# Kernel optimization log

Hardware: AMD Instinct MI355X
Metric: run time of the kernel (lower is better)

## Reference

```python
import jax, jax.numpy as jnp
import numpy as np

B, R, H, IN, L = 8, 128, 256, 512, 3
NH, DH = 4, H // 4  # attention heads


def _layernorm(x, g, b, eps=1e-5):
    mu = jnp.mean(x, axis=-1, keepdims=True)
    var = jnp.mean(jnp.square(x - mu), axis=-1, keepdims=True)
    return (x - mu) * jax.lax.rsqrt(var + eps) * g + b


def setup_inputs() -> dict:
    key = jax.random.key(0)
    ks = iter(jax.random.split(key, 40))
    s = 0.02
    d = {}
    d['x'] = jax.random.normal(next(ks), (B, IN), jnp.float32)
    d['We'] = jax.random.normal(next(ks), (IN, H), jnp.float32) * s
    d['be'] = jnp.zeros((H,), jnp.float32)
    # per-graph-layer params, stacked along leading L axis
    d['msg_W1'] = jax.random.normal(next(ks), (L, 2 * H, H), jnp.float32) * s
    d['msg_b1'] = jnp.zeros((L, H), jnp.float32)
    d['msg_W2'] = jax.random.normal(next(ks), (L, H, H), jnp.float32) * s
    d['msg_b2'] = jnp.zeros((L, H), jnp.float32)
    d['upd_W1'] = jax.random.normal(next(ks), (L, 2 * H, H), jnp.float32) * s
    d['upd_b1'] = jnp.zeros((L, H), jnp.float32)
    d['upd_W2'] = jax.random.normal(next(ks), (L, H, H), jnp.float32) * s
    d['upd_b2'] = jnp.zeros((L, H), jnp.float32)
    d['ln_g'] = jnp.ones((L, H), jnp.float32)
    d['ln_b'] = jnp.zeros((L, H), jnp.float32)
    d['rule_adj'] = jax.random.normal(next(ks), (R, R), jnp.float32)
    # multihead attention (4 heads)
    d['Wq'] = jax.random.normal(next(ks), (H, H), jnp.float32) * s
    d['bq'] = jnp.zeros((H,), jnp.float32)
    d['Wk'] = jax.random.normal(next(ks), (H, H), jnp.float32) * s
    d['bk'] = jnp.zeros((H,), jnp.float32)
    d['Wv'] = jax.random.normal(next(ks), (H, H), jnp.float32) * s
    d['bv'] = jnp.zeros((H,), jnp.float32)
    d['Wo'] = jax.random.normal(next(ks), (H, H), jnp.float32) * s
    d['bo'] = jnp.zeros((H,), jnp.float32)
    # readout MLP -> num_rules logits
    d['ro_W1'] = jax.random.normal(next(ks), (H, H), jnp.float32) * s
    d['ro_b1'] = jnp.zeros((H,), jnp.float32)
    d['ro_W2'] = jax.random.normal(next(ks), (H, R), jnp.float32) * s
    d['ro_b2'] = jnp.zeros((R,), jnp.float32)
    return d


def reference(x, We, be, msg_W1, msg_b1, msg_W2, msg_b2,
              upd_W1, upd_b1, upd_W2, upd_b2, ln_g, ln_b, rule_adj,
              Wq, bq, Wk, bk, Wv, bv, Wo, bo,
              ro_W1, ro_b1, ro_W2, ro_b2):
    # node encoder, broadcast to all rule-graph nodes: [B,R,H]
    h0 = x @ We + be
    h = jnp.broadcast_to(h0[:, None, :], (B, R, H))
    # rule adjacency with self-edges excluded (loop used i != j)
    A = jax.nn.sigmoid(rule_adj) * (1.0 - jnp.eye(R, dtype=rule_adj.dtype))  # [R,R]
    for l in range(L):
        # message_net(cat(h_i, h_j)) = relu(h_i@W1a + h_j@W1b + b1)@W2 + b2
        W1a, W1b = msg_W1[l][:H], msg_W1[l][H:]
        a = h @ W1a   # [B,R,H] (receiver i part)
        bb = h @ W1b  # [B,R,H] (sender j part)
        pre = jax.nn.relu(a[:, :, None, :] + bb[:, None, :, :] + msg_b1[l])  # [B,R,R,H]
        m = pre @ msg_W2[l] + msg_b2[l]  # [B,R,R,H] message from j to i
        agg = jnp.einsum('bijh,ij->bih', m, A)  # weighted sum over senders j
        # update_net(cat(h, agg))
        Wu1a, Wu1b = upd_W1[l][:H], upd_W1[l][H:]
        u = jax.nn.relu(h @ Wu1a + agg @ Wu1b + upd_b1[l]) @ upd_W2[l] + upd_b2[l]
        h = _layernorm(h + u, ln_g[l], ln_b[l])
    # multihead self-attention over nodes
    q = (h @ Wq + bq).reshape(B, R, NH, DH)
    k = (h @ Wk + bk).reshape(B, R, NH, DH)
    v = (h @ Wv + bv).reshape(B, R, NH, DH)
    logits = jnp.einsum('bqhd,bkhd->bhqk', q, k) / jnp.sqrt(jnp.float32(DH))
    attn = jax.nn.softmax(logits, axis=-1)
    pooled = jnp.einsum('bhqk,bkhd->bqhd', attn, v).reshape(B, R, H) @ Wo + bo
    g = jnp.mean(pooled, axis=1)  # [B,H]
    rule_logits = jax.nn.relu(g @ ro_W1 + ro_b1) @ ro_W2 + ro_b2
    rule_probabilities = jax.nn.softmax(rule_logits, axis=-1)  # [B,R]
    return rule_probabilities
```

## Files before the change

### kernel.cpp

```cpp
#include <hip/hip_runtime.h>
#include <math.h>

constexpr int NB  = 8;
constexpr int NR  = 128;
constexpr int HID = 256;
constexpr int NIN = 512;
constexpr int DHD = 64;
constexpr size_t SZ = (size_t)NB * NR * HID;

struct KP {
    const float *x, *We, *be, *msg_W1, *msg_b1, *msg_W2, *msg_b2;
    const float *upd_W1, *upd_b1, *upd_W2, *upd_b2, *ln_g, *ln_b, *rule_adj;
    const float *Wq, *bq, *Wk, *bk, *Wv, *bv, *Wo, *bo, *ro_W1, *ro_b1, *ro_W2, *ro_b2;
    float* out;
    float *N0, *N1, *N2;
    float *aB, *bbB, *p1B;
    float *aA, *bbA, *p1A;
    float *W2u, *mb2u, *Aw, *rsum;
    float *mW1s;
    float *h0g;
    float *gacc;
    float *scratch;
};

__device__ __forceinline__ void gemm_core(
    float (&As)[16][68], float (&Bs)[16][64], int m0, int n0,
    const float* __restrict__ A, const float* __restrict__ B,
    float (&acc)[4][4])
{
    int tid = threadIdx.x;
    int ty = tid >> 4, tx = tid & 15;
    int arow = tid >> 2, acol = (tid & 3) << 2;
    int brow = tid >> 4, bcol = (tid & 15) << 2;
    int m = m0 + arow;

    float4 av = *(const float4*)&A[(size_t)m * HID + acol];
    float4 bv = *(const float4*)&B[(size_t)brow * HID + n0 + bcol];

    for (int k0 = 0; k0 < HID; k0 += 16) {
        As[acol + 0][arow] = av.x;
        As[acol + 1][arow] = av.y;
        As[acol + 2][arow] = av.z;
        As[acol + 3][arow] = av.w;
        *(float4*)&Bs[brow][bcol] = bv;
        __syncthreads();
        if (k0 + 16 < HID) {
            av = *(const float4*)&A[(size_t)m * HID + k0 + 16 + acol];
            bv = *(const float4*)&B[(size_t)(k0 + 16 + brow) * HID + n0 + bcol];
        }
#pragma unroll
        for (int kk = 0; kk < 16; ++kk) {
            float4 af = *(const float4*)&As[kk][ty << 2];
            float4 bf = *(const float4*)&Bs[kk][tx << 2];
            float a_[4] = {af.x, af.y, af.z, af.w};
            float b_[4] = {bf.x, bf.y, bf.z, bf.w};
#pragma unroll
            for (int i = 0; i < 4; ++i)
#pragma unroll
                for (int j = 0; j < 4; ++j) acc[i][j] += a_[i] * b_[j];
        }
        __syncthreads();
    }
}

__device__ __forceinline__ void gemv256w(
    const float* xs, const float* __restrict__ W,
    const float* __restrict__ bias, int relu, float* ys, float* red)
{
    int tid = threadIdx.x;
    int w = tid >> 6, l = tid & 63;
    float4 acc = {0.f, 0.f, 0.f, 0.f};
    const float* Wp = W + (size_t)(w * 64) * HID + l * 4;
    const float* xp = xs + w * 64;
#pragma unroll 16
    for (int kk = 0; kk < 64; ++kk) {
        float xv = xp[kk];
        float4 wv = *(const float4*)(Wp + (size_t)kk * HID);
        acc.x += xv * wv.x; acc.y += xv * wv.y;
        acc.z += xv * wv.z; acc.w += xv * wv.w;
    }
    *(float4*)&red[w * 256 + l * 4] = acc;
    __syncthreads();
    float v = red[tid] + red[256 + tid] + red[512 + tid] + red[768 + tid];
    if (bias) v += bias[tid];
    if (relu) v = fmaxf(v, 0.0f);
    ys[tid] = v;
    __syncthreads();
}

__device__ __forceinline__ void rows4_q(
    const float (&rows)[4][HID], const float* __restrict__ W,
    int col, int q, float o[4])
{
    o[0] = o[1] = o[2] = o[3] = 0.f;
    int kb = q * 64;
#pragma unroll 4
    for (int k0 = 0; k0 < 64; k0 += 4) {
        int k = kb + k0;
        float w0 = W[(size_t)(k + 0) * HID + col];
        float w1 = W[(size_t)(k + 1) * HID + col];
        float w2 = W[(size_t)(k + 2) * HID + col];
        float w3 = W[(size_t)(k + 3) * HID + col];
#pragma unroll
        for (int ii = 0; ii < 4; ++ii) {
            float4 rv = *(const float4*)&rows[ii][k];
            o[ii] += rv.x * w0 + rv.y * w1 + rv.z * w2 + rv.w * w3;
        }
    }
}

__device__ __forceinline__ float gemv_q(
    const float* xs, const float* __restrict__ W, int col, int q)
{
    float o = 0.f;
    int kb = q * 64;
#pragma unroll 8
    for (int k = 0; k < 64; ++k)
        o += xs[kb + k] * W[(size_t)(kb + k) * HID + col];
    return o;
}

__device__ __forceinline__ void ln_stats4_q(
    float (&sred)[4][4][2], float (&mi)[4][2], const float v[4], int q)
{
    if (q == 0) {
        int w = threadIdx.x >> 6, l = threadIdx.x & 63;
        float s[4], qq[4];
#pragma unroll
        for (int ii = 0; ii < 4; ++ii) { s[ii] = v[ii]; qq[ii] = v[ii] * v[ii]; }
#pragma unroll
        for (int off = 32; off; off >>= 1) {
#pragma unroll
            for (int ii = 0; ii < 4; ++ii) {
                s[ii] += __shfl_xor(s[ii], off);
                qq[ii] += __shfl_xor(qq[ii], off);
            }
        }
        if (l == 0) {
#pragma unroll
            for (int ii = 0; ii < 4; ++ii) { sred[w][ii][0] = s[ii]; sred[w][ii][1] = qq[ii]; }
        }
    }
    __syncthreads();
    if (threadIdx.x < 4) {
        int r = threadIdx.x;
        float ss = sred[0][r][0] + sred[1][r][0] + sred[2][r][0] + sred[3][r][0];
        float qq = sred[0][r][1] + sred[1][r][1] + sred[2][r][1] + sred[3][r][1];
        float mu = ss * (1.0f / HID);
        mi[r][0] = mu;
        mi[r][1] = rsqrtf(qq * (1.0f / HID) - mu * mu + 1e-5f);
    }
    __syncthreads();
}

__global__ __launch_bounds__(256) void setup0_kernel(KP P) {
    __shared__ union {
        struct { float As[16][68]; float Bs[16][64]; } g;
        struct { float xs[NIN]; float part[8][32]; } e;
    } L;
    int blk = blockIdx.x;
    int t = threadIdx.x;

    if (blk < 32) {
        int rr = blk * 4 + (t >> 6);
        int l = t & 63;
        float s_loc = 0.f;
#pragma unroll
        for (int rep = 0; rep < 2; ++rep) {
            int j = l + rep * 64;
            float xv = P.rule_adj[rr * NR + j];
            float sg = 1.0f / (1.0f + expf(-xv));
            if (j == rr) sg = 0.0f;
            P.Aw[rr * NR + j] = sg;
            s_loc += sg;
        }
#pragma unroll
        for (int off = 32; off; off >>= 1) s_loc += __shfl_xor(s_loc, off);
        if (l == 0) P.rsum[rr] = s_loc;
    } else if (blk < 80) {
        int idx = blk - 32, l2 = idx >> 4, t16 = idx & 15;
        int m0 = (t16 >> 2) * 64, n0 = (t16 & 3) * 64;
        float acc[4][4] = {};
        gemm_core(L.g.As, L.g.Bs, m0, n0,
                  P.msg_W2 + (size_t)l2 * HID * HID,
                  P.upd_W1 + (size_t)l2 * 2 * HID * HID + (size_t)HID * HID,
                  acc);
        int ty = t >> 4, tx = t & 15;
        float* C = P.W2u + (size_t)l2 * HID * HID;
#pragma unroll
        for (int i = 0; i < 4; ++i) {
            int m = m0 + (ty << 2) + i, n = n0 + (tx << 2);
            float4 o = {acc[i][0], acc[i][1], acc[i][2], acc[i][3]};
            *(float4*)&C[(size_t)m * HID + n] = o;
        }
    } else if (blk < 83) {
        int l2 = blk - 80;
        const float* b2v = P.msg_b2 + l2 * HID;
        const float* Bm = P.upd_W1 + (size_t)l2 * 2 * HID * HID + (size_t)HID * HID;
        float acc = 0.f;
#pragma unroll 4
        for (int k = 0; k < HID; ++k) acc += b2v[k] * Bm[(size_t)k * HID + t];
        P.mb2u[l2 * HID + t] = acc;
    } else if (blk < 147) {
        int idx = blk - 83;
        int b = idx >> 3, s = idx & 7;
        L.e.xs[t]       = P.x[b * NIN + t];
        L.e.xs[256 + t] = P.x[b * NIN + 256 + t];
        __syncthreads();
        int c = t & 31, seg = t >> 5;
        int col = s * 32 + c;
        const float* Wp = P.We + (size_t)(seg * 64) * HID + col;
        const float* xp = L.e.xs + seg * 64;
        float acc = 0.f;
#pragma unroll 16
        for (int k = 0; k < 64; ++k) acc += xp[k] * Wp[(size_t)k * HID];
        L.e.part[seg][c] = acc;
        __syncthreads();
        if (t < 32) {
            float v = 0.f;
#pragma unroll
            for (int sg = 0; sg < 8; ++sg) v += L.e.part[sg][t];
            int cc = s * 32 + t;
            P.h0g[b * HID + cc] = v + P.be[cc];
        }
    } else if (blk < 163) {
        int base = (blk - 147) * 4096;
        for (int i = t; i < 4096; i += 256) {
            int o = base + i;
            P.mW1s[o] = P.msg_W1[o] + P.msg_W1[65536 + o];
        }
    } else {
        int pfid = blk - 163, npf = 256 - 163;
        const float* arr[11] = {P.We, P.msg_W1, P.msg_W2, P.upd_W1, P.upd_W2,
                                P.Wq, P.Wk, P.Wv, P.Wo, P.ro_W1, P.ro_W2};
        const int n4[11] = {32768, 98304, 49152, 98304, 49152,
                            16384, 16384, 16384, 16384, 16384, 8192};
        float s = 0.f;
        for (int a = 0; a < 11; ++a) {
            const float4* p4 = (const float4*)arr[a];
            for (int i = pfid * 256 + t; i < n4[a]; i += npf * 256) {
                float4 v = p4[i];
                s += v.x + v.y + v.z + v.w;
            }
        }
        if (s == 1.0e37f) P.scratch[pfid] = s;
    }
}

__global__ __launch_bounds__(1024) void layer0p_kernel(KP P) {
    __shared__ float h0s[HID], p0s[HID], c0s[HID], c1s[HID];
    __shared__ float u1s[4][HID];
    __shared__ float nrm[4][HID];
    __shared__ float part4[4][4][HID];
    __shared__ float sred[4][4][2];
    __shared__ float mi[4][2];
    int blk = blockIdx.x;
    int m0 = blk * 4;
    int b = m0 >> 7, i0 = m0 & 127;
    int t = threadIdx.x;
    int col = t & 255, q = t >> 8;

    if (q == 0) h0s[col] = P.h0g[b * HID + col];
    __syncthreads();

    part4[q][0][col] = gemv_q(h0s, P.upd_W1, col, q);
    part4[q][1][col] = gemv_q(h0s, P.mW1s, col, q);
    __syncthreads();
    if (q == 0) {
        c0s[col] = part4[0][0][col] + part4[1][0][col] + part4[2][0][col] + part4[3][0][col];
        float pv = part4[0][1][col] + part4[1][1][col] + part4[2][1][col] + part4[3][1][col];
        p0s[col] = fmaxf(pv + P.msg_b1[col], 0.0f);
    }
    __syncthreads();
    part4[q][0][col] = gemv_q(p0s, P.W2u, col, q);
    __syncthreads();
    if (q == 0) {
        c1s[col] = part4[0][0][col] + part4[1][0][col] + part4[2][0][col] + part4[3][0][col]
                 + P.mb2u[col];
        float ubv = P.upd_b1[col];
#pragma unroll
        for (int ii = 0; ii < 4; ++ii)
            u1s[ii][col] = fmaxf(c0s[col] + P.rsum[i0 + ii] * c1s[col] + ubv, 0.0f);
    }
    __syncthreads();

    float o[4];
    rows4_q(u1s, P.upd_W2, col, q, o);
#pragma unroll
    for (int ii = 0; ii < 4; ++ii) part4[q][ii][col] = o[ii];
    __syncthreads();
    float v[4] = {0.f, 0.f, 0.f, 0.f};
    if (q == 0) {
        float h0v = h0s[col] + P.upd_b2[col];
#pragma unroll
        for (int ii = 0; ii < 4; ++ii)
            v[ii] = part4[0][ii][col] + part4[1][ii][col] + part4[2][ii][col]
                  + part4[3][ii][col] + h0v;
    }
    ln_stats4_q(sred, mi, v, q);
    if (q == 0) {
        float gv = P.ln_g[col], btv = P.ln_b[col];
#pragma unroll
        for (int ii = 0; ii < 4; ++ii) {
            float nv = (v[ii] - mi[ii][0]) * mi[ii][1] * gv + btv;
            nrm[ii][col] = nv;
            P.N0[(size_t)(m0 + ii) * HID + col] = nv;
        }
    }
    __syncthreads();

    const float* mW1a1 = P.msg_W1 + (size_t)1 * 2 * HID * HID;
    const float* uW1a1 = P.upd_W1 + (size_t)1 * 2 * HID * HID;
    const float* pw[3] = {mW1a1, mW1a1 + (size_t)HID * HID, uW1a1};
    float* po[3] = {P.aB, P.bbB, P.p1B};
#pragma unroll
    for (int p = 0; p < 3; ++p) {
        rows4_q(nrm, pw[p], col, q, o);
#pragma unroll
        for (int ii = 0; ii < 4; ++ii) part4[q][ii][col] = o[ii];
        __syncthreads();
        if (q == 0) {
#pragma unroll
            for (int ii = 0; ii < 4; ++ii)
                po[p][(size_t)(m0 + ii) * HID + col] =
                    part4[0][ii][col] + part4[1][ii][col] +
                    part4[2][ii][col] + part4[3][ii][col];
        }
        __syncthreads();
    }
}

__global__ __launch_bounds__(1024) void aggproj_kernel(
    const float* __restrict__ a, const float* __restrict__ bbv,
    const float* __restrict__ mb1, const float* __restrict__ Aw,
    const float* __restrict__ rsumv,
    const float* __restrict__ P1, const float* __restrict__ W2u,
    const float* __restrict__ mb2u, const float* __restrict__ ub1,
    const float* __restrict__ uW2, const float* __restrict__ ub2,
    const float* __restrict__ Nprev, const float* __restrict__ lng,
    const float* __restrict__ lnb, float* __restrict__ Nout,
    const float* __restrict__ pw0, const float* __restrict__ pb0, float* __restrict__ o0,
    const float* __restrict__ pw1, const float* __restrict__ pb1, float* __restrict__ o1,
    const float* __restrict__ pw2, const float* __restrict__ pb2, float* __restrict__ o2,
    float* __restrict__ gzero)
{
    __shared__ float ap[4][HID];
    __shared__ float u1s[4][HID];
    __shared__ float nrm[4][HID];
    __shared__ float awr[4][NR];
    __shared__ float part4[4][4][HID];
    __shared__ float sred[4][4][2];
    __shared__ float mi[4][2];
    int blk = blockIdx.x;
    int b  = blk >> 5;
    int i0 = (blk & 31) * 4;
    int m0 = b * NR + i0;
    int t  = threadIdx.x;
    int col = t & 255, q = t >> 8;

    if (gzero && blk == 0 && q == 0) {
#pragma unroll
        for (int i = 0; i < 8; ++i) gzero[i * 256 + col] = 0.f;
    }

    if (t < 512) awr[t >> 7][t & 127] = Aw[(i0 + (t >> 7)) * NR + (t & 127)];

    float bias = mb1[col];
    float ai[4];
#pragma unroll
    for (int ii = 0; ii < 4; ++ii)
        ai[ii] = a[(size_t)(m0 + ii) * HID + col] + bias;
    __syncthreads();

    {
        float acc[4] = {0.f, 0.f, 0.f, 0.f};
        const float* bbb = &bbv[(size_t)b * NR * HID + col];
        int jb = q * 32;
#pragma unroll 4
        for (int j = 0; j < 32; ++j) {
            float bj = bbb[(size_t)(jb + j) * HID];
#pragma unroll
            for (int ii = 0; ii < 4; ++ii) {
                float pre = fmaxf(ai[ii] + bj, 0.0f);
                acc[ii] += awr[ii][jb + j] * pre;
            }
        }
#pragma unroll
        for (int ii = 0; ii < 4; ++ii) part4[q][ii][col] = acc[ii];
        __syncthreads();
        if (q == 0) {
#pragma unroll
            for (int ii = 0; ii < 4; ++ii)
                ap[ii][col] = part4[0][ii][col] + part4[1][ii][col]
                            + part4[2][ii][col] + part4[3][ii][col];
        }
        __syncthreads();
    }

    {
        float o[4];
        rows4_q(ap, W2u, col, q, o);
#pragma unroll
        for (int ii = 0; ii < 4; ++ii) part4[q][ii][col] = o[ii];
        __syncthreads();
        if (q == 0) {
            float mbv = mb2u[col], ubv = ub1[col];
#pragma unroll
            for (int ii = 0; ii < 4; ++ii) {
                float w2f = part4[0][ii][col] + part4[1][ii][col]
                          + part4[2][ii][col] + part4[3][ii][col];
                float vv = w2f + P1[(size_t)(m0 + ii) * HID + col]
                         + rsumv[i0 + ii] * mbv + ubv;
                u1s[ii][col] = fmaxf(vv, 0.0f);
            }
        }
        __syncthreads();
    }

    {
        float o[4];
        rows4_q(u1s, uW2, col, q, o);
#pragma unroll
        for (int ii = 0; ii < 4; ++ii) part4[q][ii][col] = o[ii];
        __syncthreads();
        float v[4] = {0.f, 0.f, 0.f, 0.f};
        if (q == 0) {
            float ub2v = ub2[col];
#pragma unroll
            for (int ii = 0; ii < 4; ++ii) {
                float uf = part4[0][ii][col] + part4[1][ii][col]
                         + part4[2][ii][col] + part4[3][ii][col];
                v[ii] = Nprev[(size_t)(m0 + ii) * HID + col] + uf + ub2v;
            }
        }
        ln_stats4_q(sred, mi, v, q);
        if (q == 0) {
            float gv = lng[col], btv = lnb[col];
#pragma unroll
            for (int ii = 0; ii < 4; ++ii) {
                float nv = (v[ii] - mi[ii][0]) * mi[ii][1] * gv + btv;
                nrm[ii][col] = nv;
                Nout[(size_t)(m0 + ii) * HID + col] = nv;
            }
        }
        __syncthreads();
    }

    {
        const float* pw[3] = {pw0, pw1, pw2};
        const float* pb[3] = {pb0, pb1, pb2};
        float* po[3] = {o0, o1, o2};
#pragma unroll
        for (int p = 0; p < 3; ++p) {
            float o[4];
            rows4_q(nrm, pw[p], col, q, o);
#pragma unroll
            for (int ii = 0; ii < 4; ++ii) part4[q][ii][col] = o[ii];
            __syncthreads();
            if (q == 0) {
                float pbv = pb[p] ? pb[p][col] : 0.f;
#pragma unroll
                for (int ii = 0; ii < 4; ++ii)
                    po[p][(size_t)(m0 + ii) * HID + col] =
                        part4[0][ii][col] + part4[1][ii][col] +
                        part4[2][ii][col] + part4[3][ii][col] + pbv;
            }
            __syncthreads();
        }
    }
}

__global__ __launch_bounds__(256) void attention_kernel(
    const float* __restrict__ q, const float* __restrict__ k,
    const float* __restrict__ v, float* __restrict__ gacc)
{
    __shared__ struct { float KhT[64][128]; float S[16][128]; float qs[16][64]; } L;
    int blk = blockIdx.x;
    int bh = blk >> 3, ig = blk & 7;
    int b = bh >> 2, hd = bh & 3;
    int i0 = ig * 16;
    int t = threadIdx.x;
    const float* qg = q + ((size_t)b * NR) * HID + hd * DHD;
    const float* kg = k + ((size_t)b * NR) * HID + hd * DHD;
    const float* vg = v + ((size_t)b * NR) * HID + hd * DHD;

    {
        int j = t >> 1, half = t & 1;
        const float* krow = kg + (size_t)j * HID + half * 32;
#pragma unroll
        for (int c = 0; c < 32; c += 4) {
            float4 kv = *(const float4*)(krow + c);
            L.KhT[half * 32 + c + 0][j] = kv.x;
            L.KhT[half * 32 + c + 1][j] = kv.y;
            L.KhT[half * 32 + c + 2][j] = kv.z;
            L.KhT[half * 32 + c + 3][j] = kv.w;
        }
    }
    {
        int ii = t >> 4, d0 = (t & 15) * 4;
        *(float4*)&L.qs[ii][d0] = *(const float4*)(qg + (size_t)(i0 + ii) * HID + d0);
    }
    __syncthreads();
    {
        int j = t & 127, ii2 = t >> 7;
        float acc[8] = {0.f,0.f,0.f,0.f,0.f,0.f,0.f,0.f};
#pragma unroll 4
        for (int d = 0; d < 64; ++d) {
            float kv = L.KhT[d][j];
#pragma unroll
            for (int ii = 0; ii < 8; ++ii) acc[ii] += L.qs[ii2 * 8 + ii][d] * kv;
        }
#pragma unroll
        for (int ii = 0; ii < 8; ++ii) L.S[ii2 * 8 + ii][j] = acc[ii] * 0.125f;
    }
    __syncthreads();
    {
        int w = t >> 6, l = t & 63;
#pragma unroll
        for (int r = w * 4; r < w * 4 + 4; ++r) {
            float e0 = L.S[r][l], e1 = L.S[r][l + 64];
            float mx = fmaxf(e0, e1);
#pragma unroll
            for (int off = 32; off; off >>= 1) mx = fmaxf(mx, __shfl_xor(mx, off));
            e0 = expf(e0 - mx); e1 = expf(e1 - mx);
            float sm = e0 + e1;
#pragma unroll
            for (int off = 32; off; off >>= 1) sm += __shfl_xor(sm, off);
            float inv = 1.0f / sm;
            L.S[r][l] = e0 * inv; L.S[r][l + 64] = e1 * inv;
        }
    }
    __syncthreads();
    {
        int d = t & 63, ir = t >> 6;
        float accv[4] = {0.f, 0.f, 0.f, 0.f};
        const float* vp = vg + d;
#pragma unroll 8
        for (int j = 0; j < NR; ++j) {
            float vv = vp[(size_t)j * HID];
#pragma unroll
            for (int p = 0; p < 4; ++p) accv[p] += L.S[p * 4 + ir][j] * vv;
        }
        float s = accv[0] + accv[1] + accv[2] + accv[3];
        atomicAdd(&gacc[b * HID + hd * DHD + d], s);
    }
}

__global__ __launch_bounds__(256) void tailf_kernel(KP P) {
    __shared__ float v0[HID], v1[HID], v2[HID];
    __shared__ float red[1024];
    int b = blockIdx.x;
    int t = threadIdx.x;
    int w = t >> 6, l = t & 63;

    v0[t] = P.gacc[b * HID + t] * (1.0f / NR);
    __syncthreads();
    gemv256w(v0, P.Wo, P.bo, 0, v1, red);
    gemv256w(v1, P.ro_W1, P.ro_b1, 1, v2, red);

    {
        float2 acc = {0.f, 0.f};
        const float* Wp = P.ro_W2 + (size_t)(w * 64) * NR + l * 2;
        const float* xp = v2 + w * 64;
#pragma unroll 8
        for (int kk = 0; kk < 64; ++kk) {
            float xv = xp[kk];
            float2 wv = *(const float2*)(Wp + (size_t)kk * NR);
            acc.x += xv * wv.x; acc.y += xv * wv.y;
        }
        *(float2*)&red[w * 128 + l * 2] = acc;
        __syncthreads();
    }
    float logit = -1e30f;
    if (t < NR) logit = red[t] + red[128 + t] + red[256 + t] + red[384 + t] + P.ro_b2[t];
    __syncthreads();
    float m = logit;
#pragma unroll
    for (int off = 32; off; off >>= 1) m = fmaxf(m, __shfl_xor(m, off));
    if (l == 0) red[w] = m;
    __syncthreads();
    m = fmaxf(red[0], red[1]);
    float e = (t < NR) ? expf(logit - m) : 0.0f;
    float ssum = e;
#pragma unroll
    for (int off = 32; off; off >>= 1) ssum += __shfl_xor(ssum, off);
    if (l == 0) red[4 + w] = ssum;
    __syncthreads();
    float tot = red[4] + red[5];
    if (t < NR) P.out[b * NR + t] = e / tot;
}

extern "C" void kernel_launch(void* const* d_in, const int* in_sizes, int n_in,
                              void* d_out, int out_size, void* d_ws, size_t ws_size,
                              hipStream_t stream)
{
    KP P;
    P.x        = (const float*)d_in[0];
    P.We       = (const float*)d_in[1];
    P.be       = (const float*)d_in[2];
    P.msg_W1   = (const float*)d_in[3];
    P.msg_b1   = (const float*)d_in[4];
    P.msg_W2   = (const float*)d_in[5];
    P.msg_b2   = (const float*)d_in[6];
    P.upd_W1   = (const float*)d_in[7];
    P.upd_b1   = (const float*)d_in[8];
    P.upd_W2   = (const float*)d_in[9];
    P.upd_b2   = (const float*)d_in[10];
    P.ln_g     = (const float*)d_in[11];
    P.ln_b     = (const float*)d_in[12];
    P.rule_adj = (const float*)d_in[13];
    P.Wq       = (const float*)d_in[14];
    P.bq       = (const float*)d_in[15];
    P.Wk       = (const float*)d_in[16];
    P.bk       = (const float*)d_in[17];
    P.Wv       = (const float*)d_in[18];
    P.bv       = (const float*)d_in[19];
    P.Wo       = (const float*)d_in[20];
    P.bo       = (const float*)d_in[21];
    P.ro_W1    = (const float*)d_in[22];
    P.ro_b1    = (const float*)d_in[23];
    P.ro_W2    = (const float*)d_in[24];
    P.ro_b2    = (const float*)d_in[25];
    P.out      = (float*)d_out;

    float* b0 = (float*)d_ws;
    P.N0     = b0;  b0 += SZ;
    P.N1     = b0;  b0 += SZ;
    P.N2     = b0;  b0 += SZ;
    P.aB     = b0;  b0 += SZ;
    P.bbB    = b0;  b0 += SZ;
    P.p1B    = b0;  b0 += SZ;
    P.aA     = b0;  b0 += SZ;
    P.bbA    = b0;  b0 += SZ;
    P.p1A    = b0;  b0 += SZ;
    P.W2u    = b0;  b0 += 3 * HID * HID;
    P.mb2u   = b0;  b0 += 3 * HID;
    P.mW1s   = b0;  b0 += HID * HID;
    P.Aw     = b0;  b0 += NR * NR;
    P.rsum   = b0;  b0 += NR;
    P.h0g    = b0;  b0 += NB * HID;
    P.gacc   = b0;  b0 += NB * HID;
    P.scratch= b0;  b0 += 256;

    setup0_kernel<<<dim3(256), 256, 0, stream>>>(P);

    layer0p_kernel<<<dim3(256), 1024, 0, stream>>>(P);

    {
        const int l = 1;
        const float* mW1a2 = P.msg_W1 + (size_t)2 * 2 * HID * HID;
        const float* uW1a2 = P.upd_W1 + (size_t)2 * 2 * HID * HID;
        aggproj_kernel<<<dim3(256), 1024, 0, stream>>>(
            P.aB, P.bbB, P.msg_b1 + (size_t)l * HID, P.Aw, P.rsum,
            P.p1B, P.W2u + (size_t)l * HID * HID, P.mb2u + l * HID,
            P.upd_b1 + (size_t)l * HID,
            P.upd_W2 + (size_t)l * HID * HID, P.upd_b2 + (size_t)l * HID,
            P.N0, P.ln_g + (size_t)l * HID, P.ln_b + (size_t)l * HID, P.N1,
            mW1a2, nullptr, P.aA,
            mW1a2 + (size_t)HID * HID, nullptr, P.bbA,
            uW1a2, nullptr, P.p1A,
            nullptr);
    }

    {
        const int l = 2;
        aggproj_kernel<<<dim3(256), 1024, 0, stream>>>(
            P.aA, P.bbA, P.msg_b1 + (size_t)l * HID, P.Aw, P.rsum,
            P.p1A, P.W2u + (size_t)l * HID * HID, P.mb2u + l * HID,
            P.upd_b1 + (size_t)l * HID,
            P.upd_W2 + (size_t)l * HID * HID, P.upd_b2 + (size_t)l * HID,
            P.N1, P.ln_g + (size_t)l * HID, P.ln_b + (size_t)l * HID, P.N2,
            P.Wq, P.bq, P.aB,
            P.Wk, P.bk, P.bbB,
            P.Wv, P.bv, P.p1B,
            P.gacc);
    }

    attention_kernel<<<dim3(256), 256, 0, stream>>>(P.aB, P.bbB, P.p1B, P.gacc);

    tailf_kernel<<<dim3(8), 256, 0, stream>>>(P);
}
```

Measured before the change: 228.1 us.

## Retile layer kernels to 2 rows x 2 columns per thread with fused projections

Restructures layer0p and aggproj kernels from 4 rows per 1024-thread block to 2 rows per 512-thread block, doubling grid size to 512 blocks. Each thread now computes two adjacent columns using float2 weight loads, and the three output projections are computed in a single pass sharing row loads, with one barrier instead of three. All threads now take part in reductions and layernorm instead of only a quarter of them. The aim is better occupancy across CUs and fewer barriers. The cost is that each weight matrix is reused over only 2 rows per block, so weight traffic from cache doubles.

Result: slower. 293.2 us (+28.5%).

```diff
diff --git a/kernel.cpp b/kernel.cpp
--- a/kernel.cpp
+++ b/kernel.cpp
@@ -88,69 +88,74 @@
     __syncthreads();
 }
 
-__device__ __forceinline__ void rows4_q(
-    const float (&rows)[4][HID], const float* __restrict__ W,
-    int col, int q, float o[4])
-{
-    o[0] = o[1] = o[2] = o[3] = 0.f;
+__device__ __forceinline__ void rows2x2_q(
+    const float (&rows)[2][HID], const float* __restrict__ W,
+    int col2, int q, float o[2][2])
+{
+    o[0][0] = o[0][1] = o[1][0] = o[1][1] = 0.f;
+    int kb = q * 64;
+#pragma unroll 8
+    for (int k0 = 0; k0 < 64; k0 += 4) {
+        int k = kb + k0;
+        float2 w0 = *(const float2*)&W[(size_t)(k + 0) * HID + col2];
+        float2 w1 = *(const float2*)&W[(size_t)(k + 1) * HID + col2];
+        float2 w2 = *(const float2*)&W[(size_t)(k + 2) * HID + col2];
+        float2 w3 = *(const float2*)&W[(size_t)(k + 3) * HID + col2];
+#pragma unroll
+        for (int ii = 0; ii < 2; ++ii) {
+            float4 rv = *(const float4*)&rows[ii][k];
+            o[ii][0] += rv.x * w0.x + rv.y * w1.x + rv.z * w2.x + rv.w * w3.x;
+            o[ii][1] += rv.x * w0.y + rv.y * w1.y + rv.z * w2.y + rv.w * w3.y;
+        }
+    }
+}
+
+__device__ __forceinline__ void rows2x2_q3(
+    const float (&rows)[2][HID],
+    const float* __restrict__ W0, const float* __restrict__ W1,
+    const float* __restrict__ W2m, int col2, int q, float o[3][2][2])
+{
+#pragma unroll
+    for (int p = 0; p < 3; ++p)
+        o[p][0][0] = o[p][0][1] = o[p][1][0] = o[p][1][1] = 0.f;
     int kb = q * 64;
 #pragma unroll 4
     for (int k0 = 0; k0 < 64; k0 += 4) {
         int k = kb + k0;
-        float w0 = W[(size_t)(k + 0) * HID + col];
-        float w1 = W[(size_t)(k + 1) * HID + col];
-        float w2 = W[(size_t)(k + 2) * HID + col];
-        float w3 = W[(size_t)(k + 3) * HID + col];
-#pragma unroll
-        for (int ii = 0; ii < 4; ++ii) {
-            float4 rv = *(const float4*)&rows[ii][k];
-            o[ii] += rv.x * w0 + rv.y * w1 + rv.z * w2 + rv.w * w3;
-        }
-    }
-}
-
-__device__ __forceinline__ float gemv_q(
-    const float* xs, const float* __restrict__ W, int col, int q)
-{
-    float o = 0.f;
+        float4 r0 = *(const float4*)&rows[0][k];
+        float4 r1 = *(const float4*)&rows[1][k];
+        const float* Wp[3] = {W0, W1, W2m};
+#pragma unroll
+        for (int p = 0; p < 3; ++p) {
+            const float* W = Wp[p];
+            float2 w0 = *(const float2*)&W[(size_t)(k + 0) * HID + col2];
+            float2 w1 = *(const float2*)&W[(size_t)(k + 1) * HID + col2];
+            float2 w2 = *(const float2*)&W[(size_t)(k + 2) * HID + col2];
+            float2 w3 = *(const float2*)&W[(size_t)(k + 3) * HID + col2];
+            o[p][0][0] += r0.x * w0.x + r0.y * w1.x + r0.z * w2.x + r0.w * w3.x;
+            o[p][0][1] += r0.x * w0.y + r0.y * w1.y + r0.z * w2.y + r0.w * w3.y;
+            o[p][1][0] += r1.x * w0.x + r1.y * w1.x + r1.z * w2.x + r1.w * w3.x;
+            o[p][1][1] += r1.x * w0.y + r1.y * w1.y + r1.z * w2.y + r1.w * w3.y;
+        }
+    }
+}
+
+__device__ __forceinline__ void row1x2_q(
+    const float* xs, const float* __restrict__ W, int col2, int q, float o[2])
+{
+    o[0] = o[1] = 0.f;
     int kb = q * 64;
 #pragma unroll 8
-    for (int k = 0; k < 64; ++k)
-        o += xs[kb + k] * W[(size_t)(kb + k) * HID + col];
-    return o;
-}
-
-__device__ __forceinline__ void ln_stats4_q(
-    float (&sred)[4][4][2], float (&mi)[4][2], const float v[4], int q)
-{
-    if (q == 0) {
-        int w = threadIdx.x >> 6, l = threadIdx.x & 63;
-        float s[4], qq[4];
-#pragma unroll
-        for (int ii = 0; ii < 4; ++ii) { s[ii] = v[ii]; qq[ii] = v[ii] * v[ii]; }
-#pragma unroll
-        for (int off = 32; off; off >>= 1) {
-#pragma unroll
-            for (int ii = 0; ii < 4; ++ii) {
-                s[ii] += __shfl_xor(s[ii], off);
-                qq[ii] += __shfl_xor(qq[ii], off);
-            }
-        }
-        if (l == 0) {
-#pragma unroll
-            for (int ii = 0; ii < 4; ++ii) { sred[w][ii][0] = s[ii]; sred[w][ii][1] = qq[ii]; }
-        }
-    }
-    __syncthreads();
-    if (threadIdx.x < 4) {
-        int r = threadIdx.x;
-        float ss = sred[0][r][0] + sred[1][r][0] + sred[2][r][0] + sred[3][r][0];
-        float qq = sred[0][r][1] + sred[1][r][1] + sred[2][r][1] + sred[3][r][1];
-        float mu = ss * (1.0f / HID);
-        mi[r][0] = mu;
-        mi[r][1] = rsqrtf(qq * (1.0f / HID) - mu * mu + 1e-5f);
-    }
-    __syncthreads();
+    for (int k0 = 0; k0 < 64; k0 += 4) {
+        int k = kb + k0;
+        float4 xv = *(const float4*)&xs[k];
+        float2 w0 = *(const float2*)&W[(size_t)(k + 0) * HID + col2];
+        float2 w1 = *(const float2*)&W[(size_t)(k + 1) * HID + col2];
+        float2 w2 = *(const float2*)&W[(size_t)(k + 2) * HID + col2];
+        float2 w3 = *(const float2*)&W[(size_t)(k + 3) * HID + col2];
+        o[0] += xv.x * w0.x + xv.y * w1.x + xv.z * w2.x + xv.w * w3.x;
+        o[1] += xv.x * w0.y + xv.y * w1.y + xv.z * w2.y + xv.w * w3.y;
+    }
 }
 
 __global__ __launch_bounds__(256) void setup0_kernel(KP P) {
@@ -247,90 +252,103 @@
     }
 }
 
-__global__ __launch_bounds__(1024) void layer0p_kernel(KP P) {
+__global__ __launch_bounds__(512) void layer0p_kernel(KP P) {
     __shared__ float h0s[HID], p0s[HID], c0s[HID], c1s[HID];
-    __shared__ float u1s[4][HID];
-    __shared__ float nrm[4][HID];
-    __shared__ float part4[4][4][HID];
-    __shared__ float sred[4][4][2];
-    __shared__ float mi[4][2];
+    __shared__ float u1s[2][HID];
+    __shared__ float nrm[2][HID];
+    __shared__ float part3[3][4][2][HID];
+    __shared__ float sred[8][2];
+    __shared__ float mi[2][2];
     int blk = blockIdx.x;
-    int m0 = blk * 4;
+    int m0 = blk * 2;
     int b = m0 >> 7, i0 = m0 & 127;
     int t = threadIdx.x;
-    int col = t & 255, q = t >> 8;
-
-    if (q == 0) h0s[col] = P.h0g[b * HID + col];
-    __syncthreads();
-
-    part4[q][0][col] = gemv_q(h0s, P.upd_W1, col, q);
-    part4[q][1][col] = gemv_q(h0s, P.mW1s, col, q);
-    __syncthreads();
-    if (q == 0) {
-        c0s[col] = part4[0][0][col] + part4[1][0][col] + part4[2][0][col] + part4[3][0][col];
-        float pv = part4[0][1][col] + part4[1][1][col] + part4[2][1][col] + part4[3][1][col];
-        p0s[col] = fmaxf(pv + P.msg_b1[col], 0.0f);
-    }
-    __syncthreads();
-    part4[q][0][col] = gemv_q(p0s, P.W2u, col, q);
-    __syncthreads();
-    if (q == 0) {
-        c1s[col] = part4[0][0][col] + part4[1][0][col] + part4[2][0][col] + part4[3][0][col]
-                 + P.mb2u[col];
-        float ubv = P.upd_b1[col];
-#pragma unroll
-        for (int ii = 0; ii < 4; ++ii)
-            u1s[ii][col] = fmaxf(c0s[col] + P.rsum[i0 + ii] * c1s[col] + ubv, 0.0f);
-    }
-    __syncthreads();
-
-    float o[4];
-    rows4_q(u1s, P.upd_W2, col, q, o);
-#pragma unroll
-    for (int ii = 0; ii < 4; ++ii) part4[q][ii][col] = o[ii];
-    __syncthreads();
-    float v[4] = {0.f, 0.f, 0.f, 0.f};
-    if (q == 0) {
-        float h0v = h0s[col] + P.upd_b2[col];
-#pragma unroll
-        for (int ii = 0; ii < 4; ++ii)
-            v[ii] = part4[0][ii][col] + part4[1][ii][col] + part4[2][ii][col]
-                  + part4[3][ii][col] + h0v;
-    }
-    ln_stats4_q(sred, mi, v, q);
-    if (q == 0) {
-        float gv = P.ln_g[col], btv = P.ln_b[col];
-#pragma unroll
-        for (int ii = 0; ii < 4; ++ii) {
-            float nv = (v[ii] - mi[ii][0]) * mi[ii][1] * gv + btv;
-            nrm[ii][col] = nv;
-            P.N0[(size_t)(m0 + ii) * HID + col] = nv;
-        }
-    }
-    __syncthreads();
-
-    const float* mW1a1 = P.msg_W1 + (size_t)1 * 2 * HID * HID;
-    const float* uW1a1 = P.upd_W1 + (size_t)1 * 2 * HID * HID;
-    const float* pw[3] = {mW1a1, mW1a1 + (size_t)HID * HID, uW1a1};
-    float* po[3] = {P.aB, P.bbB, P.p1B};
-#pragma unroll
-    for (int p = 0; p < 3; ++p) {
-        rows4_q(nrm, pw[p], col, q, o);
-#pragma unroll
-        for (int ii = 0; ii < 4; ++ii) part4[q][ii][col] = o[ii];
-        __syncthreads();
-        if (q == 0) {
-#pragma unroll
-            for (int ii = 0; ii < 4; ++ii)
-                po[p][(size_t)(m0 + ii) * HID + col] =
-                    part4[0][ii][col] + part4[1][ii][col] +
-                    part4[2][ii][col] + part4[3][ii][col];
-        }
-        __syncthreads();
-    }
-}
-
-__global__ __launch_bounds__(1024) void aggproj_kernel(
+    int c2 = t & 127, q = t >> 7, col2 = c2 * 2;
+    int r = t >> 8, c = t & 255;
+
+    if (t < 256) h0s[t] = P.h0g[b * HID + t];
+    __syncthreads();
+
+    {
+        float o0v[2], o1v[2];
+        row1x2_q(h0s, P.upd_W1, col2, q, o0v);
+        row1x2_q(h0s, P.mW1s, col2, q, o1v);
+        *(float2*)&part3[0][q][0][col2] = make_float2(o0v[0], o0v[1]);
+        *(float2*)&part3[0][q][1][col2] = make_float2(o1v[0], o1v[1]);
+        __syncthreads();
+        float s = part3[0][0][r][c] + part3[0][1][r][c]
+                + part3[0][2][r][c] + part3[0][3][r][c];
+        if (r == 0) c0s[c] = s;
+        else        p0s[c] = fmaxf(s + P.msg_b1[c], 0.0f);
+        __syncthreads();
+    }
+    {
+        float ov[2];
+        row1x2_q(p0s, P.W2u, col2, q, ov);
+        *(float2*)&part3[0][q][0][col2] = make_float2(ov[0], ov[1]);
+        __syncthreads();
+        if (t < 256)
+            c1s[t] = part3[0][0][0][t] + part3[0][1][0][t]
+                   + part3[0][2][0][t] + part3[0][3][0][t] + P.mb2u[t];
+        __syncthreads();
+    }
+    u1s[r][c] = fmaxf(c0s[c] + P.rsum[i0 + r] * c1s[c] + P.upd_b1[c], 0.0f);
+    __syncthreads();
+
+    {
+        float o[2][2];
+        rows2x2_q(u1s, P.upd_W2, col2, q, o);
+#pragma unroll
+        for (int ii = 0; ii < 2; ++ii)
+            *(float2*)&part3[0][q][ii][col2] = make_float2(o[ii][0], o[ii][1]);
+        __syncthreads();
+        float uf = part3[0][0][r][c] + part3[0][1][r][c]
+                 + part3[0][2][r][c] + part3[0][3][r][c];
+        float v = h0s[c] + uf + P.upd_b2[c];
+        float s = v, qq = v * v;
+#pragma unroll
+        for (int off = 32; off; off >>= 1) {
+            s += __shfl_xor(s, off); qq += __shfl_xor(qq, off);
+        }
+        int wid = t >> 6;
+        if ((t & 63) == 0) { sred[wid][0] = s; sred[wid][1] = qq; }
+        __syncthreads();
+        if (t < 2) {
+            float ss = sred[4*t][0] + sred[4*t+1][0] + sred[4*t+2][0] + sred[4*t+3][0];
+            float q2 = sred[4*t][1] + sred[4*t+1][1] + sred[4*t+2][1] + sred[4*t+3][1];
+            float mu = ss * (1.0f / HID);
+            mi[t][0] = mu;
+            mi[t][1] = rsqrtf(q2 * (1.0f / HID) - mu * mu + 1e-5f);
+        }
+        __syncthreads();
+        float nv = (v - mi[r][0]) * mi[r][1] * P.ln_g[c] + P.ln_b[c];
+        nrm[r][c] = nv;
+        P.N0[(size_t)(m0 + r) * HID + c] = nv;
+        __syncthreads();
+    }
+
+    {
+        const float* mW1a1 = P.msg_W1 + (size_t)1 * 2 * HID * HID;
+        const float* uW1a1 = P.upd_W1 + (size_t)1 * 2 * HID * HID;
+        float o[3][2][2];
+        rows2x2_q3(nrm, mW1a1, mW1a1 + (size_t)HID * HID, uW1a1, col2, q, o);
+#pragma unroll
+        for (int p = 0; p < 3; ++p)
+#pragma unroll
+            for (int ii = 0; ii < 2; ++ii)
+                *(float2*)&part3[p][q][ii][col2] = make_float2(o[p][ii][0], o[p][ii][1]);
+        __syncthreads();
+        float* po[3] = {P.aB, P.bbB, P.p1B};
+#pragma unroll
+        for (int p = 0; p < 3; ++p) {
+            float s = part3[p][0][r][c] + part3[p][1][r][c]
+                    + part3[p][2][r][c] + part3[p][3][r][c];
+            po[p][(size_t)(m0 + r) * HID + c] = s;
+        }
+    }
+}
+
+__global__ __launch_bounds__(512) void aggproj_kernel(
     const float* __restrict__ a, const float* __restrict__ bbv,
     const float* __restrict__ mb1, const float* __restrict__ Aw,
     const float* __restrict__ rsumv,
@@ -344,128 +362,122 @@
     const float* __restrict__ pw2, const float* __restrict__ pb2, float* __restrict__ o2,
     float* __restrict__ gzero)
 {
-    __shared__ float ap[4][HID];
-    __shared__ float u1s[4][HID];
-    __shared__ float nrm[4][HID];
-    __shared__ float awr[4][NR];
-    __shared__ float part4[4][4][HID];
-    __shared__ float sred[4][4][2];
-    __shared__ float mi[4][2];
+    __shared__ float awr[2][NR];
+    __shared__ float ap[2][HID];
+    __shared__ float u1s[2][HID];
+    __shared__ float nrm[2][HID];
+    __shared__ float part3[3][4][2][HID];
+    __shared__ float sred[8][2];
+    __shared__ float mi[2][2];
     int blk = blockIdx.x;
-    int b  = blk >> 5;
-    int i0 = (blk & 31) * 4;
+    int b  = blk >> 6;
+    int i0 = (blk & 63) * 2;
     int m0 = b * NR + i0;
     int t  = threadIdx.x;
-    int col = t & 255, q = t >> 8;
-
-    if (gzero && blk == 0 && q == 0) {
-#pragma unroll
-        for (int i = 0; i < 8; ++i) gzero[i * 256 + col] = 0.f;
-    }
-
-    if (t < 512) awr[t >> 7][t & 127] = Aw[(i0 + (t >> 7)) * NR + (t & 127)];
-
-    float bias = mb1[col];
-    float ai[4];
-#pragma unroll
-    for (int ii = 0; ii < 4; ++ii)
-        ai[ii] = a[(size_t)(m0 + ii) * HID + col] + bias;
-    __syncthreads();
-
-    {
-        float acc[4] = {0.f, 0.f, 0.f, 0.f};
-        const float* bbb = &bbv[(size_t)b * NR * HID + col];
+    int c2 = t & 127, q = t >> 7, col2 = c2 * 2;
+    int r = t >> 8, c = t & 255;
+
+    if (gzero && blk == 0) {
+#pragma unroll
+        for (int i = 0; i < 4; ++i) gzero[i * 512 + t] = 0.f;
+    }
+
+    if (t < 256) awr[t >> 7][t & 127] = Aw[(i0 + (t >> 7)) * NR + (t & 127)];
+
+    float2 bi = *(const float2*)&mb1[col2];
+    float2 ai[2];
+#pragma unroll
+    for (int ii = 0; ii < 2; ++ii) {
+        float2 av = *(const float2*)&a[(size_t)(m0 + ii) * HID + col2];
+        ai[ii].x = av.x + bi.x; ai[ii].y = av.y + bi.y;
+    }
+    __syncthreads();
+
+    {
+        float acc[2][2] = {{0.f, 0.f}, {0.f, 0.f}};
+        const float* bbb = &bbv[(size_t)b * NR * HID + col2];
         int jb = q * 32;
 #pragma unroll 4
         for (int j = 0; j < 32; ++j) {
-            float bj = bbb[(size_t)(jb + j) * HID];
-#pragma unroll
-            for (int ii = 0; ii < 4; ++ii) {
-                float pre = fmaxf(ai[ii] + bj, 0.0f);
-                acc[ii] += awr[ii][jb + j] * pre;
-            }
-        }
-#pragma unroll
-        for (int ii = 0; ii < 4; ++ii) part4[q][ii][col] = acc[ii];
-        __syncthreads();
-        if (q == 0) {
-#pragma unroll
-            for (int ii = 0; ii < 4; ++ii)
-                ap[ii][col] = part4[0][ii][col] + part4[1][ii][col]
-                            + part4[2][ii][col] + part4[3][ii][col];
-        }
-        __syncthreads();
-    }
-
-    {
-        float o[4];
-        rows4_q(ap, W2u, col, q, o);
-#pragma unroll
-        for (int ii = 0; ii < 4; ++ii) part4[q][ii][col] = o[ii];
-        __syncthreads();
-        if (q == 0) {
-            float mbv = mb2u[col], ubv = ub1[col];
-#pragma unroll
-            for (int ii = 0; ii < 4; ++ii) {
-                float w2f = part4[0][ii][col] + part4[1][ii][col]
-                          + part4[2][ii][col] + part4[3][ii][col];
-                float vv = w2f + P1[(size_t)(m0 + ii) * HID + col]
-                         + rsumv[i0 + ii] * mbv + ubv;
-                u1s[ii][col] = fmaxf(vv, 0.0f);
-            }
-        }
-        __syncthreads();
-    }
-
-    {
-        float o[4];
-        rows4_q(u1s, uW2, col, q, o);
-#pragma unroll
-        for (int ii = 0; ii < 4; ++ii) part4[q][ii][col] = o[ii];
-        __syncthreads();
-        float v[4] = {0.f, 0.f, 0.f, 0.f};
-        if (q == 0) {
-            float ub2v = ub2[col];
-#pragma unroll
-            for (int ii = 0; ii < 4; ++ii) {
-                float uf = part4[0][ii][col] + part4[1][ii][col]
-                         + part4[2][ii][col] + part4[3][ii][col];
-                v[ii] = Nprev[(size_t)(m0 + ii) * HID + col] + uf + ub2v;
-            }
-        }
-        ln_stats4_q(sred, mi, v, q);
-        if (q == 0) {
-            float gv = lng[col], btv = lnb[col];
-#pragma unroll
-            for (int ii = 0; ii < 4; ++ii) {
-                float nv = (v[ii] - mi[ii][0]) * mi[ii][1] * gv + btv;
-                nrm[ii][col] = nv;
-                Nout[(size_t)(m0 + ii) * HID + col] = nv;
-            }
-        }
-        __syncthreads();
-    }
-
-    {
-        const float* pw[3] = {pw0, pw1, pw2};
+            float2 bj = *(const float2*)&bbb[(size_t)(jb + j) * HID];
+            float w0 = awr[0][jb + j], w1 = awr[1][jb + j];
+            float p00 = fmaxf(ai[0].x + bj.x, 0.f), p01 = fmaxf(ai[0].y + bj.y, 0.f);
+            float p10 = fmaxf(ai[1].x + bj.x, 0.f), p11 = fmaxf(ai[1].y + bj.y, 0.f);
+            acc[0][0] += w0 * p00; acc[0][1] += w0 * p01;
+            acc[1][0] += w1 * p10; acc[1][1] += w1 * p11;
+        }
+        *(float2*)&part3[0][q][0][col2] = make_float2(acc[0][0], acc[0][1]);
+        *(float2*)&part3[0][q][1][col2] = make_float2(acc[1][0], acc[1][1]);
+        __syncthreads();
+        ap[r][c] = part3[0][0][r][c] + part3[0][1][r][c]
+                 + part3[0][2][r][c] + part3[0][3][r][c];
+        __syncthreads();
+    }
+
+    {
+        float o[2][2];
+        rows2x2_q(ap, W2u, col2, q, o);
+#pragma unroll
+        for (int ii = 0; ii < 2; ++ii)
+            *(float2*)&part3[0][q][ii][col2] = make_float2(o[ii][0], o[ii][1]);
+        __syncthreads();
+        float w2f = part3[0][0][r][c] + part3[0][1][r][c]
+                  + part3[0][2][r][c] + part3[0][3][r][c];
+        float vv = w2f + P1[(size_t)(m0 + r) * HID + c]
+                 + rsumv[i0 + r] * mb2u[c] + ub1[c];
+        u1s[r][c] = fmaxf(vv, 0.0f);
+        __syncthreads();
+    }
+
+    {
+        float o[2][2];
+        rows2x2_q(u1s, uW2, col2, q, o);
+#pragma unroll
+        for (int ii = 0; ii < 2; ++ii)
+            *(float2*)&part3[0][q][ii][col2] = make_float2(o[ii][0], o[ii][1]);
+        __syncthreads();
+        float uf = part3[0][0][r][c] + part3[0][1][r][c]
+                 + part3[0][2][r][c] + part3[0][3][r][c];
+        float v = Nprev[(size_t)(m0 + r) * HID + c] + uf + ub2[c];
+        float s = v, qq = v * v;
+#pragma unroll
+        for (int off = 32; off; off >>= 1) {
+            s += __shfl_xor(s, off); qq += __shfl_xor(qq, off);
+        }
+        int wid = t >> 6;
+        if ((t & 63) == 0) { sred[wid][0] = s; sred[wid][1] = qq; }
+        __syncthreads();
+        if (t < 2) {
+            float ss = sred[4*t][0] + sred[4*t+1][0] + sred[4*t+2][0] + sred[4*t+3][0];
+            float q2 = sred[4*t][1] + sred[4*t+1][1] + sred[4*t+2][1] + sred[4*t+3][1];
+            float mu = ss * (1.0f / HID);
+            mi[t][0] = mu;
+            mi[t][1] = rsqrtf(q2 * (1.0f / HID) - mu * mu + 1e-5f);
+        }
+        __syncthreads();
+        float nv = (v - mi[r][0]) * mi[r][1] * lng[c] + lnb[c];
+        nrm[r][c] = nv;
+        Nout[(size_t)(m0 + r) * HID + c] = nv;
+        __syncthreads();
+    }
+
+    {
+        float o[3][2][2];
+        rows2x2_q3(nrm, pw0, pw1, pw2, col2, q, o);
+#pragma unroll
+        for (int p = 0; p < 3; ++p)
+#pragma unroll
+            for (int ii = 0; ii < 2; ++ii)
+                *(float2*)&part3[p][q][ii][col2] = make_float2(o[p][ii][0], o[p][ii][1]);
+        __syncthreads();
         const float* pb[3] = {pb0, pb1, pb2};
         float* po[3] = {o0, o1, o2};
 #pragma unroll
         for (int p = 0; p < 3; ++p) {
-            float o[4];
-            rows4_q(nrm, pw[p], col, q, o);
-#pragma unroll
-            for (int ii = 0; ii < 4; ++ii) part4[q][ii][col] = o[ii];
-            __syncthreads();
-            if (q == 0) {
-                float pbv = pb[p] ? pb[p][col] : 0.f;
-#pragma unroll
-                for (int ii = 0; ii < 4; ++ii)
-                    po[p][(size_t)(m0 + ii) * HID + col] =
-                        part4[0][ii][col] + part4[1][ii][col] +
-                        part4[2][ii][col] + part4[3][ii][col] + pbv;
-            }
-            __syncthreads();
+            float s = part3[p][0][r][c] + part3[p][1][r][c]
+                    + part3[p][2][r][c] + part3[p][3][r][c];
+            if (pb[p]) s += pb[p][c];
+            po[p][(size_t)(m0 + r) * HID + c] = s;
         }
     }
 }
@@ -644,13 +656,13 @@
 
     setup0_kernel<<<dim3(256), 256, 0, stream>>>(P);
 
-    layer0p_kernel<<<dim3(256), 1024, 0, stream>>>(P);
+    layer0p_kernel<<<dim3(512), 512, 0, stream>>>(P);
 
     {
         const int l = 1;
         const float* mW1a2 = P.msg_W1 + (size_t)2 * 2 * HID * HID;
         const float* uW1a2 = P.upd_W1 + (size_t)2 * 2 * HID * HID;
-        aggproj_kernel<<<dim3(256), 1024, 0, stream>>>(
+        aggproj_kernel<<<dim3(512), 512, 0, stream>>>(
             P.aB, P.bbB, P.msg_b1 + (size_t)l * HID, P.Aw, P.rsum,
             P.p1B, P.W2u + (size_t)l * HID * HID, P.mb2u + l * HID,
             P.upd_b1 + (size_t)l * HID,
@@ -664,7 +676,7 @@
 
     {
         const int l = 2;
-        aggproj_kernel<<<dim3(256), 1024, 0, stream>>>(
+        aggproj_kernel<<<dim3(512), 512, 0, stream>>>(
             P.aA, P.bbA, P.msg_b1 + (size_t)l * HID, P.Aw, P.rsum,
             P.p1A, P.W2u + (size_t)l * HID * HID, P.mb2u + l * HID,
             P.upd_b1 + (size_t)l * HID,
```
